# Kernel optimization log

Measured on AMD Instinct MI355X. Metric: run time of the kernel, lower is better.

## Reference

```python
import jax
jax.config.update("jax_enable_x64", True)
import jax.numpy as jnp
import numpy as np

# --- Field setup -------------------------------------------------------------
# The original uses BLS12-381 Fr (255-bit Montgomery limbs). JAX has no native
# 256-bit ints, so the reference uses an NTT-friendly 31-bit prime with the
# same algorithmic structure (two-adic radix-2 INTT, grand products, MSM-style
# commitment reduction). Products of two residues fit in int64.
P = 2013265921          # 15 * 2^27 + 1, two-adicity 27
G = 31                  # generator of F_P^*
LOG_N = 20
N = 1 << LOG_N
W = pow(G, (P - 1) // N, P)      # primitive N-th root of unity
W_INV = pow(W, P - 2, P)
N_INV = pow(N, P - 2, P)
K1, K2, K3 = 7, 13, 17           # PLONK coset shifts for wire identities


def _bitrev_perm(n):
    logn = n.bit_length() - 1
    idx = np.arange(n, dtype=np.int64)
    rev = np.zeros(n, dtype=np.int64)
    for i in range(logn):
        rev = (rev << 1) | ((idx >> i) & 1)
    return rev


def _twiddles(n, root):
    logn = n.bit_length() - 1
    out = []
    for s in range(1, logn + 1):
        m = 1 << s
        wm = pow(root, n // m, P)
        half = m >> 1
        ws = np.empty(half, dtype=np.int64)
        w = 1
        for k in range(half):
            ws[k] = w
            w = (w * wm) % P
        out.append(jnp.asarray(ws))
    return out

_BREV = jnp.asarray(_bitrev_perm(N))
_TW_INV = _twiddles(N, W_INV)


def _ntt_core(a, tw):
    # iterative radix-2 Cooley-Tukey, fully vectorized per stage
    n = a.shape[0]
    a = a[_BREV]
    for s, ws in enumerate(tw):
        half = 1 << s
        a = a.reshape(-1, 2 * half)         # [n/(2*half), 2*half]
        u = a[:, :half]
        t = (a[:, half:] * ws[None, :]) % P
        a = jnp.concatenate([(u + t) % P, (u - t) % P], axis=1)
    return a.reshape(n)


def intt(evals):
    # inverse NTT: evaluations on the domain -> coefficients (nn.Intt)
    return (_ntt_core(evals, _TW_INV) * N_INV) % P


def inv_mod(x):
    # batch modular inverse: x^(P-2), exponent is a compile-time constant
    e = P - 2
    res = jnp.ones_like(x)
    base = x % P
    while e:
        if e & 1:
            res = (res * base) % P
        base = (base * base) % P
        e >>= 1
    return res


def cumprod_mod(x):
    return jax.lax.associative_scan(lambda a, b: (a * b) % P, x)


def shifted_cumprod(r):
    # z[0] = 1, z[i] = prod_{j<i} r[j]
    c = cumprod_mod(r)
    return jnp.concatenate([jnp.ones((1,), r.dtype), c[:-1]])


def commit(poly, ck):
    # stand-in for the KZG MSM: <poly, ck> mod P (same reduction structure)
    return jnp.sum((poly * ck) % P) % P


def perm_z(wires, sigmas, beta, gamma, omega_pows):
    # PLONK copy-constraint grand product (mod.compute_permutation_poly)
    ids = (omega_pows, (K1 * omega_pows) % P,
           (K2 * omega_pows) % P, (K3 * omega_pows) % P)
    num = jnp.ones((N,), jnp.int64)
    den = jnp.ones((N,), jnp.int64)
    for w, i, s in zip(wires, ids, sigmas):
        num = (num * ((w + (beta * i) % P + gamma) % P)) % P
        den = (den * ((w + (beta * s) % P + gamma) % P)) % P
    return shifted_cumprod((num * inv_mod(den)) % P)


def lookup_z2(f, t, h1, h2, delta, epsilon):
    # plookup grand product (mod.compute_lookup_permutation_poly)
    one_plus_d = (1 + delta) % P
    ep1d = (epsilon * one_plus_d) % P
    t_next = jnp.roll(t, -1)
    h1_next = jnp.roll(h1, -1)
    h2_next = jnp.roll(h2, -1)
    num = (one_plus_d * ((epsilon + f) % P)) % P
    num = (num * ((ep1d + t + (delta * t_next) % P) % P)) % P
    a = (ep1d + h1 + (delta * h1_next) % P) % P
    b = (ep1d + h2 + (delta * h2_next) % P) % P
    den = (a * b) % P
    return shifted_cumprod((num * inv_mod(den)) % P)


def setup_inputs() -> dict:
    key = jax.random.key(0)
    ks = jax.random.split(key, 16)
    def ri(k):
        return jax.random.randint(k, (N,), 0, P, dtype=jnp.int64)
    return {
        "w_l": ri(ks[0]), "w_r": ri(ks[1]), "w_o": ri(ks[2]), "w_4": ri(ks[3]),
        "q_lookup": jax.random.randint(ks[4], (N,), 0, 2, dtype=jnp.int64),
        "t1": ri(ks[5]), "t2": ri(ks[6]), "t3": ri(ks[7]), "t4": ri(ks[8]),
        "sigma_l": ri(ks[9]), "sigma_r": ri(ks[10]),
        "sigma_o": ri(ks[11]), "sigma_4": ri(ks[12]),
        "ck": ri(ks[13]),
        "zeta": 123457, "beta": 98765, "gamma": 54321,
        "delta": 13579, "epsilon": 24680,
    }


def reference(w_l, w_r, w_o, w_4, q_lookup, t1, t2, t3, t4,
              sigma_l, sigma_r, sigma_o, sigma_4, ck,
              zeta, beta, gamma, delta, epsilon):
    z2c = (zeta * zeta) % P
    z3c = (z2c * zeta) % P
    # zkp.compress: zeta-combine lookup table columns
    t = (t1 + (zeta * t2) % P + (z2c * t3) % P + (z3c * t4) % P) % P
    table_poly = intt(t)
    # zkp.compute_query_table: compressed wire query where selector is on,
    # padded with table values where it is off
    q = (w_l + (zeta * w_r) % P + (z2c * w_o) % P + (z3c * w_4) % P) % P
    f = jnp.where(q_lookup == 1, q, t)
    f_poly = intt(f)
    # witness INTTs
    w_l_poly = intt(w_l)
    w_r_poly = intt(w_r)
    w_o_poly = intt(w_o)
    w_4_poly = intt(w_4)
    # combine_split: sorted multiset of f union t, split alternating
    s = jnp.sort(jnp.concatenate([f, t]))
    h1, h2 = s[0::2], s[1::2]
    h1_poly = intt(h1)
    h2_poly = intt(h2)
    # domain elements 1, W, W^2, ...
    omega_pows = shifted_cumprod(jnp.full((N,), W, dtype=jnp.int64))
    z = perm_z((w_l, w_r, w_o, w_4), (sigma_l, sigma_r, sigma_o, sigma_4),
               beta, gamma, omega_pows)
    z_poly = intt(z)
    z2 = lookup_z2(f, t, h1, h2, delta, epsilon)
    z2_poly = intt(z2)
    polys = (w_l_poly, w_r_poly, w_o_poly, w_4_poly, f_poly, table_poly,
             h1_poly, h2_poly, z_poly, z2_poly)
    commits = jnp.stack([commit(p, ck) for p in polys])
    return polys + (commits,)
```

## Files before the change

kernel.cpp:

```cpp
#include <hip/hip_runtime.h>
#include <stdint.h>

#define PRIME 2013265921u
#define LOGN  20
#define NN    (1u << LOGN)

static constexpr uint64_t cpowmod(uint64_t b, uint64_t e){
  uint64_t r = 1; b %= PRIME;
  while (e){ if (e & 1) r = r * b % PRIME; b = b * b % PRIME; e >>= 1; }
  return r;
}
static constexpr uint32_t WFWD = (uint32_t)cpowmod(31u, (PRIME - 1u) >> LOGN);
static constexpr uint32_t WINV = (uint32_t)cpowmod(WFWD, PRIME - 2u);
static constexpr uint32_t NINV = (uint32_t)cpowmod(NN, PRIME - 2u);
static constexpr uint64_t MBAR = 0xFFFFFFFFFFFFFFFFull / PRIME;

__device__ uint32_t g_U[1024];
__device__ uint32_t g_V[1024];
__device__ uint2    g_TWp[1024];
__device__ uint2    g_U2p[1024];
__device__ uint32_t g_bcnt[2048];
__device__ uint32_t g_boff[2048];
__device__ uint32_t g_bcur[2048];
__device__ uint32_t g_btot[2048];
__device__ uint32_t g_bpre[2048];
__device__ unsigned long long g_commit[10];

__device__ __forceinline__ uint32_t mulmod(uint32_t a, uint32_t b){
  uint64_t t = (uint64_t)a * b;
  uint32_t q = (uint32_t)__umul64hi(t, MBAR);
  uint32_t r = (uint32_t)t - q * PRIME;
  if (r >= PRIME) r -= PRIME;
  return r;
}
__device__ __forceinline__ uint32_t shoup_mul(uint32_t a, uint32_t w, uint32_t ws){
  uint32_t q = __umulhi(a, ws);
  uint32_t r = a * w - q * PRIME;
  if (r >= PRIME) r -= PRIME;
  return r;
}
__device__ __forceinline__ uint32_t addmod(uint32_t a, uint32_t b){
  uint32_t s = a + b; return (s >= PRIME) ? s - PRIME : s;
}
__device__ __forceinline__ uint32_t submod(uint32_t a, uint32_t b){
  return (a >= b) ? (a - b) : (a + (PRIME - b));
}
__device__ __forceinline__ uint32_t addmod3(uint32_t a, uint32_t b, uint32_t c){
  return addmod(addmod(a, b), c);
}
__device__ __forceinline__ uint32_t powmod_dev(uint32_t b, uint32_t e){
  uint32_t r = 1u;
  while (e){ if (e & 1u) r = mulmod(r, b); b = mulmod(b, b); e >>= 1u; }
  return r;
}

__global__ __launch_bounds__(1024) void k_zero(){
  const uint32_t t = blockIdx.x * 1024u + threadIdx.x;
  if (t < 2048u) g_bcnt[t] = 0u;
  if (t < 10u)   g_commit[t] = 0ull;
}

__global__ __launch_bounds__(1024) void k_tables(){
  const uint32_t i = threadIdx.x;
  if (blockIdx.x == 0){
    g_U[i] = powmod_dev(WINV, i);
  } else if (blockIdx.x == 1){
    g_V[i] = powmod_dev(WINV, i << 10);
  } else if (blockIdx.x == 2){
    const uint32_t w = mulmod(NINV, powmod_dev(WINV, i));
    g_U2p[i] = make_uint2(w, (uint32_t)((((uint64_t)w) << 32) / PRIME));
  } else {
    uint32_t j;
    if      (i < 512u)  j = i;
    else if (i < 768u)  j = (i - 512u)  << 1;
    else if (i < 896u)  j = (i - 768u)  << 2;
    else if (i < 960u)  j = (i - 896u)  << 3;
    else if (i < 992u)  j = (i - 960u)  << 4;
    else if (i < 1008u) j = (i - 992u)  << 5;
    else if (i < 1016u) j = (i - 1008u) << 6;
    else if (i < 1020u) j = (i - 1016u) << 7;
    else if (i < 1022u) j = (i - 1020u) << 8;
    else                j = 0u;
    const uint32_t w = powmod_dev(WINV, j << 10);
    g_TWp[i] = make_uint2(w, (uint32_t)((((uint64_t)w) << 32) / PRIME));
  }
}

__global__ __launch_bounds__(1024) void k_elemA(
    const uint32_t* __restrict__ wl, const uint32_t* __restrict__ wr,
    const uint32_t* __restrict__ wo, const uint32_t* __restrict__ w4,
    const uint32_t* __restrict__ ql, const uint32_t* __restrict__ x1,
    const uint32_t* __restrict__ x2, const uint32_t* __restrict__ x3,
    const uint32_t* __restrict__ x4, const uint32_t* __restrict__ zeta_p,
    uint32_t* __restrict__ o32)
{
  __shared__ uint32_t hcnt[2048];
  const int t = threadIdx.x;
  hcnt[t] = 0u; hcnt[t + 1024] = 0u;
  __syncthreads();

  const uint32_t zeta = zeta_p[0];
  const uint32_t zc2 = mulmod(zeta, zeta), zc3 = mulmod(zc2, zeta);
  const uint32_t i0 = (uint32_t)blockIdx.x * 4096u + (uint32_t)t * 4u;

  uint4 vt1 = *(const uint4*)(x1 + i0);
  uint4 vt2 = *(const uint4*)(x2 + i0);
  uint4 vt3 = *(const uint4*)(x3 + i0);
  uint4 vt4 = *(const uint4*)(x4 + i0);
  uint4 vwl = *(const uint4*)(wl + i0);
  uint4 vwr = *(const uint4*)(wr + i0);
  uint4 vwo = *(const uint4*)(wo + i0);
  uint4 vw4 = *(const uint4*)(w4 + i0);
  uint4 vql = *(const uint4*)(ql + i0);

  uint32_t T1[4] = {vt1.x, vt1.y, vt1.z, vt1.w};
  uint32_t T2[4] = {vt2.x, vt2.y, vt2.z, vt2.w};
  uint32_t T3[4] = {vt3.x, vt3.y, vt3.z, vt3.w};
  uint32_t T4[4] = {vt4.x, vt4.y, vt4.z, vt4.w};
  uint32_t L1[4] = {vwl.x, vwl.y, vwl.z, vwl.w};
  uint32_t L2[4] = {vwr.x, vwr.y, vwr.z, vwr.w};
  uint32_t L3[4] = {vwo.x, vwo.y, vwo.z, vwo.w};
  uint32_t L4[4] = {vw4.x, vw4.y, vw4.z, vw4.w};
  uint32_t QL[4] = {vql.x, vql.y, vql.z, vql.w};

  uint32_t tv[4], fv[4];
  #pragma unroll
  for (int k = 0; k < 4; ++k){
    uint32_t tt = addmod(addmod(T1[k], mulmod(zeta, T2[k])),
                         addmod(mulmod(zc2, T3[k]), mulmod(zc3, T4[k])));
    uint32_t qq = addmod(addmod(L1[k], mulmod(zeta, L2[k])),
                         addmod(mulmod(zc2, L3[k]), mulmod(zc3, L4[k])));
    tv[k] = tt; fv[k] = (QL[k] == 1u) ? qq : tt;
  }
  uint4 o;
  o.x = tv[0]; o.y = tv[1]; o.z = tv[2]; o.w = tv[3];
  *(uint4*)(o32 + 5u*NN + i0) = o;
  o.x = fv[0]; o.y = fv[1]; o.z = fv[2]; o.w = fv[3];
  *(uint4*)(o32 + 4u*NN + i0) = o;

  #pragma unroll
  for (int k = 0; k < 4; ++k){ atomicAdd(&hcnt[fv[k] >> 20], 1u);
                               atomicAdd(&hcnt[tv[k] >> 20], 1u); }
  __syncthreads();
  uint32_t c0 = hcnt[t];          if (c0) atomicAdd(&g_bcnt[t], c0);
  uint32_t c1 = hcnt[t + 1024];   if (c1) atomicAdd(&g_bcnt[t + 1024], c1);
}

__global__ __launch_bounds__(1024) void k_bscan(){
  __shared__ uint32_t SA[2048], SB[2048];
  const int t = threadIdx.x;
  SA[t] = g_bcnt[t];
  SA[t + 1024] = g_bcnt[t + 1024];
  __syncthreads();
  uint32_t* sp = SA; uint32_t* dp = SB;
  for (int off = 1; off < 2048; off <<= 1){
    for (int i = t; i < 2048; i += 1024)
      dp[i] = (i >= off) ? (sp[i - off] + sp[i]) : sp[i];
    uint32_t* tmp = sp; sp = dp; dp = tmp;
    __syncthreads();
  }
  uint32_t e0 = t ? sp[t - 1] : 0u;
  uint32_t e1 = sp[t + 1023];
  g_boff[t] = e0;         g_bcur[t] = e0;
  g_boff[t + 1024] = e1;  g_bcur[t + 1024] = e1;
}

__global__ __launch_bounds__(1024) void k_scat2(uint32_t* __restrict__ o32){
  __shared__ uint32_t sorted[8192];
  __shared__ uint32_t hist[2048];
  __shared__ uint32_t SA[2048];
  __shared__ uint32_t wsum[16];
  __shared__ uint32_t gbase[2048];
  const int t = threadIdx.x;
  const uint32_t base = blockIdx.x * 8192u;

  hist[t] = 0u; hist[t + 1024] = 0u;
  __syncthreads();

  uint32_t v[8], rk[8];
  #pragma unroll
  for (int k = 0; k < 8; ++k)
    v[k] = o32[4u*NN + base + (uint32_t)t + (uint32_t)k * 1024u];
  #pragma unroll
  for (int k = 0; k < 8; ++k)
    rk[k] = atomicAdd(&hist[v[k] >> 20], 1u);
  __syncthreads();

  const uint32_t lane = (uint32_t)t & 63u, wid = (uint32_t)t >> 6;
  const uint32_t e0 = hist[2*t], e1 = hist[2*t + 1];
  const uint32_t s = e0 + e1;
  uint32_t scan = s;
  #pragma unroll
  for (int off = 1; off < 64; off <<= 1){
    uint32_t u = __shfl_up(scan, off, 64);
    if (lane >= (uint32_t)off) scan += u;
  }
  if (lane == 63u) wsum[wid] = scan;
  __syncthreads();
  if (t < 64){
    uint32_t u = (t < 16) ? wsum[t] : 0u;
    #pragma unroll
    for (int off = 1; off < 16; off <<= 1){
      uint32_t x2 = __shfl_up(u, off, 64);
      if ((uint32_t)t >= (uint32_t)off) u += x2;
    }
    if (t < 16) wsum[t] = u;
  }
  __syncthreads();
  const uint32_t wbase = wid ? wsum[wid - 1] : 0u;
  const uint32_t incl = wbase + scan;
  SA[2*t]     = incl - e1;
  SA[2*t + 1] = incl;
  __syncthreads();
  uint32_t* sp = SA;

  for (int b = t; b < 2048; b += 1024){
    uint32_t c = hist[b];
    if (c) gbase[b] = atomicAdd(&g_bcur[b], c);
  }
  __syncthreads();

  #pragma unroll
  for (int k = 0; k < 8; ++k){
    uint32_t b = v[k] >> 20;
    uint32_t ls = b ? sp[b - 1] : 0u;
    sorted[ls + rk[k]] = v[k];
  }
  __syncthreads();

  for (int i = t; i < 8192; i += 1024){
    uint32_t vv = sorted[i];
    uint32_t b = vv >> 20;
    uint32_t ls = b ? sp[b - 1] : 0u;
    o32[6u*NN + gbase[b] + (uint32_t)i - ls] = vv;
  }
}

__global__ __launch_bounds__(256) void k_bsort(uint32_t* __restrict__ o32){
  __shared__ uint32_t sorted[2048];
  __shared__ uint32_t SA[1024], SB[1024];
  __shared__ uint32_t wsum[4];
  const int b = blockIdx.x, t = threadIdx.x;
  uint32_t n = g_bcnt[b]; if (n > 2048u) n = 2048u;
  const uint32_t off = g_boff[b];

  for (int i = t; i < 1024; i += 256) SA[i] = 0u;
  __syncthreads();

  uint32_t v[8], rk[8];
  #pragma unroll
  for (int k = 0; k < 8; ++k){
    const uint32_t i = (uint32_t)t + (uint32_t)k * 256u;
    if (i < n){
      v[k] = o32[6u*NN + off + i];
      rk[k] = atomicAdd(&SA[(v[k] >> 10) & 1023u], 1u);
    }
  }
  __syncthreads();

  const uint32_t lane = (uint32_t)t & 63u, wid = (uint32_t)t >> 6;
  const uint32_t h0 = SA[4*t], h1 = SA[4*t + 1], h2 = SA[4*t + 2], h3 = SA[4*t + 3];
  const uint32_t s = h0 + h1 + h2 + h3;
  uint32_t scan = s;
  #pragma unroll
  for (int o = 1; o < 64; o <<= 1){
    uint32_t u = __shfl_up(scan, o, 64);
    if (lane >= (uint32_t)o) scan += u;
  }
  if (lane == 63u) wsum[wid] = scan;
  __syncthreads();
  if (t < 64){
    uint32_t u = (t < 4) ? wsum[t] : 0u;
    #pragma unroll
    for (int o = 1; o < 4; o <<= 1){
      uint32_t x2 = __shfl_up(u, o, 64);
      if ((uint32_t)t >= (uint32_t)o) u += x2;
    }
    if (t < 4) wsum[t] = u;
  }
  __syncthreads();
  const uint32_t wbase = wid ? wsum[wid - 1] : 0u;
  const uint32_t incl = wbase + scan;
  SB[4*t + 3] = incl;
  SB[4*t + 2] = incl - h3;
  SB[4*t + 1] = incl - h3 - h2;
  SB[4*t + 0] = incl - h3 - h2 - h1;
  __syncthreads();
  uint32_t* sp = SB;

  #pragma unroll
  for (int k = 0; k < 8; ++k){
    const uint32_t i = (uint32_t)t + (uint32_t)k * 256u;
    if (i < n){
      const uint32_t d = (v[k] >> 10) & 1023u;
      const uint32_t s2 = d ? sp[d - 1] : 0u;
      sorted[s2 + rk[k]] = v[k];
    }
  }
  __syncthreads();

  for (int d = t; d < 1024; d += 256){
    const uint32_t s2 = d ? sp[d - 1] : 0u;
    const uint32_t e = sp[d];
    for (uint32_t i = s2 + 1; i < e; ++i){
      const uint32_t key = sorted[i];
      uint32_t j = i;
      while (j > s2 && sorted[j - 1] > key){ sorted[j] = sorted[j - 1]; --j; }
      sorted[j] = key;
    }
  }
  __syncthreads();

  for (uint32_t i = (uint32_t)t; i < n; i += 256u) o32[6u*NN + off + i] = sorted[i];
}

__global__ __launch_bounds__(256) void k_ratio(
    const uint32_t* __restrict__ wl, const uint32_t* __restrict__ wr,
    const uint32_t* __restrict__ wo, const uint32_t* __restrict__ w4,
    const uint32_t* __restrict__ sl, const uint32_t* __restrict__ sr,
    const uint32_t* __restrict__ so, const uint32_t* __restrict__ s4,
    const uint32_t* __restrict__ beta_p, const uint32_t* __restrict__ gamma_p,
    const uint32_t* __restrict__ delta_p, const uint32_t* __restrict__ eps_p,
    uint32_t* __restrict__ o32)
{
  __shared__ uint32_t SA[256], SB[256];
  const int blk = blockIdx.x, t = threadIdx.x;
  const int second = blk >> 9;
  const uint32_t base = ((uint32_t)(blk & 511) << 11) + ((uint32_t)t << 3);
  uint32_t num[8], den[8];
  if (!second){
    const uint32_t beta = beta_p[0], gamma = gamma_p[0];
    #pragma unroll
    for (int k = 0; k < 8; ++k){
      uint32_t i = base + (uint32_t)k;
      uint32_t e = (NN - i) & (NN - 1u);
      uint32_t om = mulmod(g_U[e & 1023u], g_V[e >> 10]);
      uint32_t bo = mulmod(beta, om);
      uint32_t n = addmod3(wl[i], bo, gamma);
      n = mulmod(n, addmod3(wr[i], mulmod(7u,  bo), gamma));
      n = mulmod(n, addmod3(wo[i], mulmod(13u, bo), gamma));
      n = mulmod(n, addmod3(w4[i], mulmod(17u, bo), gamma));
      uint32_t d = addmod3(wl[i], mulmod(beta, sl[i]), gamma);
      d = mulmod(d, addmod3(wr[i], mulmod(beta, sr[i]), gamma));
      d = mulmod(d, addmod3(wo[i], mulmod(beta, so[i]), gamma));
      d = mulmod(d, addmod3(w4[i], mulmod(beta, s4[i]), gamma));
      num[k] = n; den[k] = d;
    }
  } else {
    const uint32_t del = delta_p[0], ep = eps_p[0];
    const uint32_t opd = addmod(1u, del), ep1d = mulmod(ep, opd);
    #pragma unroll
    for (int k = 0; k < 8; ++k){
      uint32_t i = base + (uint32_t)k;
      uint32_t fi = o32[4u*NN + i], ti = o32[5u*NN + i];
      uint32_t tn = o32[5u*NN + ((i + 1u) & (NN - 1u))];
      uint32_t h1  = o32[6u*NN + 2u*i];
      uint32_t h2  = o32[6u*NN + 2u*i + 1u];
      uint32_t h1n = o32[6u*NN + ((2u*i + 2u) & (2u*NN - 1u))];
      uint32_t h2n = o32[6u*NN + ((2u*i + 3u) & (2u*NN - 1u))];
      uint32_t n = mulmod(opd, addmod(ep, fi));
      n = mulmod(n, addmod3(ep1d, ti, mulmod(del, tn)));
      uint32_t d = mulmod(addmod3(ep1d, h1, mulmod(del, h1n)),
                          addmod3(ep1d, h2, mulmod(del, h2n)));
      num[k] = n; den[k] = d;
    }
  }
  bool ok = true;
  #pragma unroll
  for (int k = 0; k < 8; ++k) ok = ok && (den[k] != 0u);
  uint32_t r[8];
  if (ok){
    uint32_t pp[8];
    pp[0] = den[0];
    #pragma unroll
    for (int k = 1; k < 8; ++k) pp[k] = mulmod(pp[k-1], den[k]);
    uint32_t iv = powmod_dev(pp[7], PRIME - 2u);
    #pragma unroll
    for (int k = 7; k >= 1; --k){
      r[k] = mulmod(num[k], mulmod(iv, pp[k-1]));
      iv = mulmod(iv, den[k]);
    }
    r[0] = mulmod(num[0], iv);
  } else {
    #pragma unroll
    for (int k = 0; k < 8; ++k) r[k] = mulmod(num[k], powmod_dev(den[k], PRIME - 2u));
  }
  uint32_t tp = r[0];
  #pragma unroll
  for (int k = 1; k < 8; ++k) tp = mulmod(tp, r[k]);
  SA[t] = tp; __syncthreads();
  uint32_t* sp = SA; uint32_t* dp = SB;
  for (int off = 1; off < 256; off <<= 1){
    dp[t] = (t >= off) ? mulmod(sp[t - off], sp[t]) : sp[t];
    uint32_t* tmp = sp; sp = dp; dp = tmp;
    __syncthreads();
  }
  if (t == 255) g_btot[blk] = sp[255];
  uint32_t run = t ? sp[t - 1] : 1u;
  const uint32_t zo = 8u*NN + ((uint32_t)second << 20) + base;
  #pragma unroll
  for (int k = 0; k < 8; ++k){
    o32[zo + (uint32_t)k] = run;
    run = mulmod(run, r[k]);
  }
}

__global__ __launch_bounds__(512) void k_btscan(){
  __shared__ uint32_t SA[512], SB[512];
  const int a = blockIdx.x, t = threadIdx.x;
  SA[t] = g_btot[a * 512 + t];
  __syncthreads();
  uint32_t* sp = SA; uint32_t* dp = SB;
  for (int off = 1; off < 512; off <<= 1){
    dp[t] = (t >= off) ? mulmod(sp[t - off], sp[t]) : sp[t];
    uint32_t* tmp = sp; sp = dp; dp = tmp;
    __syncthreads();
  }
  g_bpre[a * 512 + t] = t ? sp[t - 1] : 1u;
}

__global__ __launch_bounds__(256) void k_apply(uint32_t* __restrict__ o32){
  const uint32_t g = blockIdx.x * 256u + threadIdx.x;
  const uint32_t base = g << 2;
  const uint32_t m = g_bpre[base >> 11];
  uint4* zz = (uint4*)(o32 + 8u*NN);
  uint4 v = zz[g];
  v.x = mulmod(v.x, m); v.y = mulmod(v.y, m); v.z = mulmod(v.z, m); v.w = mulmod(v.w, m);
  zz[g] = v;
}

struct Desc  { const uint32_t* p; uint32_t stride; uint32_t off; };
struct Descs { Desc d[10]; };
struct Map   { int g[10]; };

#define SWZ(i, c) (((i) << 4) + ((c) ^ (((i) >> 1) & 15)))

__device__ __forceinline__ void ntt1024_reg(uint32_t x[16], int l,
                                            const uint2* __restrict__ sTW){
  #pragma unroll
  for (int st = 9; st >= 6; --st){
    const int bb = 1 << (st - 6);
    const int base = (st == 9) ? 0 : (st == 8) ? 512 : (st == 7) ? 768 : 896;
    #pragma unroll
    for (int r = 0; r < 16; ++r){
      if ((r & bb) == 0){
        const int r2 = r | bb;
        const uint32_t u = x[r], v = x[r2];
        const uint2 wv = sTW[base + ((r & (bb - 1)) << 6) + l];
        x[r]  = addmod(u, v);
        x[r2] = shoup_mul(submod(u, v), wv.x, wv.y);
      }
    }
  }
  #pragma unroll
  for (int st = 5; st >= 0; --st){
    const int h = 1 << st;
    const int base = (st == 5) ? 960 : (st == 4) ? 992 : (st == 3) ? 1008
                   : (st == 2) ? 1016 : (st == 1) ? 1020 : 1022;
    const uint2 wv = sTW[base + (l & (h - 1))];
    const bool hi = (l & h) != 0;
    #pragma unroll
    for (int r = 0; r < 16; ++r){
      const uint32_t y = __shfl_xor(x[r], h, 64);
      const uint32_t a = addmod(x[r], y);
      const uint32_t b = shoup_mul(submod(y, x[r]), wv.x, wv.y);
      x[r] = hi ? b : a;
    }
  }
}

__global__ __launch_bounds__(1024, 8) void k_intt1(Descs ds, uint32_t* __restrict__ mid){
  __shared__ uint32_t tile[16384];
  __shared__ uint2 sTW[1024];
  const int arr = blockIdx.x >> 6;
  const int c0 = (blockIdx.x & 63) << 4;
  const Desc de = ds.d[arr];
  const int t = threadIdx.x;
  sTW[t] = g_TWp[t];
  if (de.stride == 1u){
    #pragma unroll
    for (int it = 0; it < 4; ++it){
      const int row = (it << 8) + (t >> 2);
      const int cb = (t & 3) << 2;
      uint4 v = *(const uint4*)(de.p + (size_t)row * 1024u + (uint32_t)(c0 + cb));
      tile[SWZ(row, cb + 0)] = v.x; tile[SWZ(row, cb + 1)] = v.y;
      tile[SWZ(row, cb + 2)] = v.z; tile[SWZ(row, cb + 3)] = v.w;
    }
  } else {
    #pragma unroll
    for (int it = 0; it < 4; ++it){
      const int row = (it << 8) + (t >> 2);
      const int cb = (t & 3) << 2;
      const size_t b0 = 2u * ((size_t)row * 1024u + (uint32_t)(c0 + cb));
      uint4 a0 = *(const uint4*)(de.p + b0);
      uint4 a1 = *(const uint4*)(de.p + b0 + 4u);
      if (de.off == 0u){
        tile[SWZ(row, cb + 0)] = a0.x; tile[SWZ(row, cb + 1)] = a0.z;
        tile[SWZ(row, cb + 2)] = a1.x; tile[SWZ(row, cb + 3)] = a1.z;
      } else {
        tile[SWZ(row, cb + 0)] = a0.y; tile[SWZ(row, cb + 1)] = a0.w;
        tile[SWZ(row, cb + 2)] = a1.y; tile[SWZ(row, cb + 3)] = a1.w;
      }
    }
  }
  __syncthreads();
  const int w = t >> 6, l = t & 63;
  uint32_t x[16];
  #pragma unroll
  for (int r = 0; r < 16; ++r) x[r] = tile[SWZ(l + (r << 6), w)];
  ntt1024_reg(x, l, sTW);
  const uint32_t i1g = (uint32_t)(c0 + w);
  const uint32_t rl = __brev((uint32_t)l) >> 26;
  #pragma unroll
  for (int r = 0; r < 16; ++r){
    const uint32_t rr = __brev((uint32_t)r) >> 28;
    const uint32_t j1 = (rl << 4) | rr;
    const uint32_t e = j1 * i1g;
    const uint2 wa = g_U2p[e & 1023u];
    const uint32_t hv = e >> 10;
    const uint2 wb = sTW[hv & 511u];
    uint32_t wbw = wb.x, wbs = wb.y;
    if (hv & 512u){ wbw = PRIME - wbw; wbs = ~wbs; }
    x[r] = shoup_mul(x[r], wa.x, wa.y);
    x[r] = shoup_mul(x[r], wbw, wbs);
  }
  __syncthreads();
  #pragma unroll
  for (int r = 0; r < 16; ++r) tile[SWZ(l + (r << 6), w)] = x[r];
  __syncthreads();
  uint32_t* mo = mid + ((size_t)arr << 20);
  #pragma unroll
  for (int it = 0; it < 4; ++it){
    const int row = (it << 8) + (t >> 2);
    const int cb = (t & 3) << 2;
    uint4 v;
    v.x = tile[SWZ(row, cb + 0)]; v.y = tile[SWZ(row, cb + 1)];
    v.z = tile[SWZ(row, cb + 2)]; v.w = tile[SWZ(row, cb + 3)];
    *(uint4*)(mo + (size_t)row * 1024u + (uint32_t)(c0 + cb)) = v;
  }
}

__global__ __launch_bounds__(1024, 8) void k_intt2(const uint32_t* __restrict__ mid,
                                                   uint32_t* __restrict__ o32,
                                                   const uint32_t* __restrict__ ck,
                                                   Map mp){
  __shared__ uint32_t tile[16384];
  __shared__ uint2 sTW[1024];
  const int arrL = blockIdx.x >> 6;
  const int m0 = (blockIdx.x & 63) << 4;
  const int t = threadIdx.x;
  const int w = t >> 6, l = t & 63;
  const int gidx = mp.g[arrL];
  const uint32_t* mi = mid + ((size_t)arrL << 20);
  const uint32_t p = __brev((uint32_t)(m0 + w)) >> 22;
  sTW[t] = g_TWp[t];
  #pragma unroll
  for (int it = 0; it < 4; ++it){
    const int kb = (it << 8) + (l << 2);
    uint4 v = *(const uint4*)(mi + p * 1024u + (uint32_t)kb);
    tile[SWZ(kb + 0, w)] = v.x; tile[SWZ(kb + 1, w)] = v.y;
    tile[SWZ(kb + 2, w)] = v.z; tile[SWZ(kb + 3, w)] = v.w;
  }
  __syncthreads();
  uint32_t x[16];
  #pragma unroll
  for (int r = 0; r < 16; ++r) x[r] = tile[SWZ(l + (r << 6), w)];
  ntt1024_reg(x, l, sTW);
  __syncthreads();
  #pragma unroll
  for (int r = 0; r < 16; ++r) tile[SWZ(l + (r << 6), w)] = x[r];
  __syncthreads();
  unsigned long long acc = 0ull;
  uint32_t* oa = o32 + ((size_t)gidx << 20);
  #pragma unroll
  for (int it = 0; it < 4; ++it){
    const int j2 = (it << 8) + (t >> 2);
    const int rb = (t & 3) << 2;
    const uint32_t q = __brev((uint32_t)j2) >> 22;
    uint4 v;
    v.x = tile[SWZ((int)q, rb + 0)]; v.y = tile[SWZ((int)q, rb + 1)];
    v.z = tile[SWZ((int)q, rb + 2)]; v.w = tile[SWZ((int)q, rb + 3)];
    const uint32_t oi = (uint32_t)j2 * 1024u + (uint32_t)(m0 + rb);
    *(uint4*)(oa + oi) = v;
    uint4 cv = *(const uint4*)(ck + oi);
    acc += (unsigned long long)mulmod(v.x, cv.x);
    acc += (unsigned long long)mulmod(v.y, cv.y);
    acc += (unsigned long long)mulmod(v.z, cv.z);
    acc += (unsigned long long)mulmod(v.w, cv.w);
  }
  #pragma unroll
  for (int off = 32; off >= 1; off >>= 1) acc += __shfl_down(acc, off, 64);
  __syncthreads();
  unsigned long long* redw = (unsigned long long*)tile;
  if (l == 0) redw[w] = acc;
  __syncthreads();
  if (t < 64){
    unsigned long long s = (t < 16) ? redw[t] : 0ull;
    #pragma unroll
    for (int off = 8; off >= 1; off >>= 1) s += __shfl_down(s, off, 64);
    if (t == 0) atomicAdd(&g_commit[gidx], s);
  }
}

__global__ __launch_bounds__(256) void k_brev(const uint32_t* __restrict__ src,
                                              uint32_t stride, uint32_t off,
                                              uint32_t* __restrict__ dst){
  const uint32_t i = blockIdx.x * 256u + threadIdx.x;
  const uint32_t r = __brev(i) >> 12;
  dst[i] = src[(size_t)r * stride + off];
}

__global__ __launch_bounds__(1024) void k_stage09(uint32_t* __restrict__ wk){
  __shared__ uint32_t sm[1024];
  const int t = threadIdx.x;
  const uint32_t gbase = blockIdx.x * 1024u;
  sm[t] = wk[gbase + t];
  __syncthreads();
  for (int s = 0; s <= 9; ++s){
    if (t < 512){
      const int half = 1 << s;
      const int k = t & (half - 1);
      const int i0 = ((t >> s) << (s + 1)) | k;
      const int i1 = i0 + half;
      const uint32_t tw = g_V[(uint32_t)k << (9 - s)];
      const uint32_t u = sm[i0];
      const uint32_t tv = mulmod(sm[i1], tw);
      sm[i0] = addmod(u, tv);
      sm[i1] = submod(u, tv);
    }
    __syncthreads();
  }
  wk[gbase + t] = sm[t];
}

__global__ __launch_bounds__(256) void k_stage(uint32_t* __restrict__ wk, int s){
  const uint32_t q = blockIdx.x * 256u + threadIdx.x;
  const uint32_t half = 1u << s;
  const uint32_t k = q & (half - 1u);
  const uint32_t i0 = ((q >> s) << (s + 1)) | k;
  const uint32_t i1 = i0 + half;
  const uint32_t e = k << (19 - s);
  const uint32_t tw = mulmod(g_U[e & 1023u], g_V[e >> 10]);
  const uint32_t u = wk[i0];
  const uint32_t tv = mulmod(wk[i1], tw);
  wk[i0] = addmod(u, tv);
  wk[i1] = submod(u, tv);
}

__global__ __launch_bounds__(1024) void k_scale_commit(const uint32_t* __restrict__ src,
                                                       uint32_t* dst,
                                                       const uint32_t* __restrict__ ck,
                                                       int cidx){
  __shared__ unsigned long long red[1024];
  const uint32_t i = blockIdx.x * 1024u + threadIdx.x;
  const uint32_t val = mulmod(src[i], NINV);
  dst[i] = val;
  red[threadIdx.x] = (unsigned long long)mulmod(val, ck[i]);
  __syncthreads();
  for (int s = 512; s > 0; s >>= 1){
    if ((int)threadIdx.x < s) red[threadIdx.x] += red[threadIdx.x + s];
    __syncthreads();
  }
  if (threadIdx.x == 0) atomicAdd(&g_commit[cidx], red[0]);
}

__global__ void k_final(uint32_t* __restrict__ out){
  const int i = threadIdx.x;
  if (i < 10) out[(size_t)10 * NN + i] = (uint32_t)(g_commit[i] % (unsigned long long)PRIME);
}

extern "C" void kernel_launch(void* const* d_in, const int* in_sizes, int n_in,
                              void* d_out, int out_size, void* d_ws, size_t ws_size,
                              hipStream_t stream)
{
  const uint32_t* wl   = (const uint32_t*)d_in[0];
  const uint32_t* wr   = (const uint32_t*)d_in[1];
  const uint32_t* wo   = (const uint32_t*)d_in[2];
  const uint32_t* w4   = (const uint32_t*)d_in[3];
  const uint32_t* ql   = (const uint32_t*)d_in[4];
  const uint32_t* t1   = (const uint32_t*)d_in[5];
  const uint32_t* t2   = (const uint32_t*)d_in[6];
  const uint32_t* t3   = (const uint32_t*)d_in[7];
  const uint32_t* t4   = (const uint32_t*)d_in[8];
  const uint32_t* sl   = (const uint32_t*)d_in[9];
  const uint32_t* sr   = (const uint32_t*)d_in[10];
  const uint32_t* so   = (const uint32_t*)d_in[11];
  const uint32_t* s4   = (const uint32_t*)d_in[12];
  const uint32_t* ck   = (const uint32_t*)d_in[13];
  const uint32_t* zeta = (const uint32_t*)d_in[14];
  const uint32_t* beta = (const uint32_t*)d_in[15];
  const uint32_t* gam  = (const uint32_t*)d_in[16];
  const uint32_t* del  = (const uint32_t*)d_in[17];
  const uint32_t* eps  = (const uint32_t*)d_in[18];
  uint32_t* o32 = (uint32_t*)d_out;
  (void)in_sizes; (void)n_in; (void)out_size;

  k_zero  <<<2, 1024, 0, stream>>>();
  k_tables<<<4, 1024, 0, stream>>>();
  k_elemA <<<256, 1024, 0, stream>>>(wl, wr, wo, w4, ql, t1, t2, t3, t4, zeta, o32);
  k_bscan <<<1, 1024, 0, stream>>>();
  k_scat2 <<<256, 1024, 0, stream>>>(o32);
  k_bsort <<<1920, 256, 0, stream>>>(o32);
  k_ratio <<<1024, 256, 0, stream>>>(wl, wr, wo, w4, sl, sr, so, s4, beta, gam, del, eps, o32);
  k_btscan<<<2, 512, 0, stream>>>();
  k_apply <<<2048, 256, 0, stream>>>(o32);

  Desc ds[10];
  ds[0] = { wl,          1u, 0u };
  ds[1] = { wr,          1u, 0u };
  ds[2] = { wo,          1u, 0u };
  ds[3] = { w4,          1u, 0u };
  ds[4] = { o32 + 4u*NN, 1u, 0u };
  ds[5] = { o32 + 5u*NN, 1u, 0u };
  ds[6] = { o32 + 6u*NN, 2u, 0u };
  ds[7] = { o32 + 6u*NN, 2u, 1u };
  ds[8] = { o32 + 8u*NN, 1u, 0u };
  ds[9] = { o32 + 9u*NN, 1u, 0u };

  const size_t wsWords = ws_size / 4u;
  if (wsWords >= 2ull * NN){
    static const int ord[10] = {6,7, 4,5, 8,9, 0,1, 2,3};
    const int chunk = (wsWords >= 10ull * NN) ? 10 : 2;
    uint32_t* mid = (uint32_t*)d_ws;
    for (int s0 = 0; s0 < 10; s0 += chunk){
      const int cnt = (10 - s0 < chunk) ? (10 - s0) : chunk;
      Descs sub; Map mp;
      for (int a = 0; a < 10; ++a){
        const int g = ord[(a < cnt) ? s0 + a : s0];
        sub.d[a] = ds[g]; mp.g[a] = g;
      }
      k_intt1<<<64 * cnt, 1024, 0, stream>>>(sub, mid);
      k_intt2<<<64 * cnt, 1024, 0, stream>>>(mid, o32, ck, mp);
    }
  } else {
    auto run_intt = [&](const Desc& d, uint32_t workSlot, int dstSlot){
      uint32_t* wk = o32 + (size_t)workSlot * NN;
      k_brev   <<<4096, 256, 0, stream>>>(d.p, d.stride, d.off, wk);
      k_stage09<<<1024, 1024, 0, stream>>>(wk);
      for (int s = 10; s < 20; ++s)
        k_stage<<<2048, 256, 0, stream>>>(wk, s);
      k_scale_commit<<<1024, 1024, 0, stream>>>(wk, o32 + (size_t)dstSlot * NN, ck, dstSlot);
    };
    k_brev<<<4096, 256, 0, stream>>>(ds[6].p, 2u, 0u, o32 + 0u*NN);
    k_brev<<<4096, 256, 0, stream>>>(ds[7].p, 2u, 1u, o32 + 1u*NN);
    {
      uint32_t* wk0 = o32;
      uint32_t* wk1 = o32 + NN;
      k_stage09<<<1024, 1024, 0, stream>>>(wk0);
      for (int s = 10; s < 20; ++s) k_stage<<<2048, 256, 0, stream>>>(wk0, s);
      k_scale_commit<<<1024, 1024, 0, stream>>>(wk0, o32 + 6u*NN, ck, 6);
      k_stage09<<<1024, 1024, 0, stream>>>(wk1);
      for (int s = 10; s < 20; ++s) k_stage<<<2048, 256, 0, stream>>>(wk1, s);
      k_scale_commit<<<1024, 1024, 0, stream>>>(wk1, o32 + 7u*NN, ck, 7);
    }
    run_intt(ds[4], 0u, 4);
    run_intt(ds[5], 1u, 5);
    run_intt(ds[8], 0u, 8);
    run_intt(ds[9], 1u, 9);
    run_intt(ds[0], 0u, 0);
    run_intt(ds[1], 1u, 1);
    run_intt(ds[2], 2u, 2);
    run_intt(ds[3], 3u, 3);
  }
  k_final<<<1, 64, 0, stream>>>(o32);
}
```

Measured before the change: 200.0 us.

## Halve NTT block size: each thread processes two columns with half-size LDS tile

The two four-step NTT kernels now launch 512 threads instead of 1024. Each wave handles two 1024-point columns held in registers (xA/xB), and the shared tile shrinks from 64KB to 32KB, staged in two halves. The goal is to cut LDS footprint so more blocks fit per CU, and to expose more independent work per thread so latency is better hidden. In exchange, register pressure doubles, which could reduce occupancy, and the extra half-staging passes add barriers.

Result: slower. 215.5 us (+7.7%).

```diff
diff --git a/kernel.cpp b/kernel.cpp
--- a/kernel.cpp
+++ b/kernel.cpp
@@ -435,8 +435,8 @@
 
 #define SWZ(i, c) (((i) << 4) + ((c) ^ (((i) >> 1) & 15)))
 
-__device__ __forceinline__ void ntt1024_reg(uint32_t x[16], int l,
-                                            const uint2* __restrict__ sTW){
+__device__ __forceinline__ void ntt1024_reg2(uint32_t xA[16], uint32_t xB[16], int l,
+                                             const uint2* __restrict__ sTW){
   #pragma unroll
   for (int st = 9; st >= 6; --st){
     const int bb = 1 << (st - 6);
@@ -445,10 +445,13 @@
     for (int r = 0; r < 16; ++r){
       if ((r & bb) == 0){
         const int r2 = r | bb;
-        const uint32_t u = x[r], v = x[r2];
         const uint2 wv = sTW[base + ((r & (bb - 1)) << 6) + l];
-        x[r]  = addmod(u, v);
-        x[r2] = shoup_mul(submod(u, v), wv.x, wv.y);
+        const uint32_t uA = xA[r], vA = xA[r2];
+        xA[r]  = addmod(uA, vA);
+        xA[r2] = shoup_mul(submod(uA, vA), wv.x, wv.y);
+        const uint32_t uB = xB[r], vB = xB[r2];
+        xB[r]  = addmod(uB, vB);
+        xB[r2] = shoup_mul(submod(uB, vB), wv.x, wv.y);
       }
     }
   }
@@ -461,132 +464,191 @@
     const bool hi = (l & h) != 0;
     #pragma unroll
     for (int r = 0; r < 16; ++r){
-      const uint32_t y = __shfl_xor(x[r], h, 64);
-      const uint32_t a = addmod(x[r], y);
-      const uint32_t b = shoup_mul(submod(y, x[r]), wv.x, wv.y);
-      x[r] = hi ? b : a;
-    }
-  }
-}
-
-__global__ __launch_bounds__(1024, 8) void k_intt1(Descs ds, uint32_t* __restrict__ mid){
-  __shared__ uint32_t tile[16384];
+      const uint32_t yA = __shfl_xor(xA[r], h, 64);
+      const uint32_t aA = addmod(xA[r], yA);
+      const uint32_t bA = shoup_mul(submod(yA, xA[r]), wv.x, wv.y);
+      xA[r] = hi ? bA : aA;
+      const uint32_t yB = __shfl_xor(xB[r], h, 64);
+      const uint32_t aB = addmod(xB[r], yB);
+      const uint32_t bB = shoup_mul(submod(yB, xB[r]), wv.x, wv.y);
+      xB[r] = hi ? bB : aB;
+    }
+  }
+}
+
+__global__ __launch_bounds__(512, 8) void k_intt1(Descs ds, uint32_t* __restrict__ mid){
+  __shared__ uint32_t tile[8192];
   __shared__ uint2 sTW[1024];
+  const int t = threadIdx.x;
+  sTW[t] = g_TWp[t];
+  sTW[t + 512] = g_TWp[t + 512];
   const int arr = blockIdx.x >> 6;
   const int c0 = (blockIdx.x & 63) << 4;
   const Desc de = ds.d[arr];
+  const int w = t >> 6, l = t & 63;
+  uint32_t xA[16], xB[16];
+
+  #pragma unroll
+  for (int H = 0; H < 2; ++H){
+    if (H) __syncthreads();
+    if (de.stride == 1u){
+      #pragma unroll
+      for (int it = 0; it < 4; ++it){
+        const int rl = (it << 7) + (t >> 2);
+        const int cb = (t & 3) << 2;
+        const int row = (H << 9) + rl;
+        uint4 v = *(const uint4*)(de.p + (size_t)row * 1024u + (uint32_t)(c0 + cb));
+        tile[SWZ(rl, cb + 0)] = v.x; tile[SWZ(rl, cb + 1)] = v.y;
+        tile[SWZ(rl, cb + 2)] = v.z; tile[SWZ(rl, cb + 3)] = v.w;
+      }
+    } else {
+      #pragma unroll
+      for (int it = 0; it < 4; ++it){
+        const int rl = (it << 7) + (t >> 2);
+        const int cb = (t & 3) << 2;
+        const int row = (H << 9) + rl;
+        const size_t b0 = 2u * ((size_t)row * 1024u + (uint32_t)(c0 + cb));
+        uint4 a0 = *(const uint4*)(de.p + b0);
+        uint4 a1 = *(const uint4*)(de.p + b0 + 4u);
+        if (de.off == 0u){
+          tile[SWZ(rl, cb + 0)] = a0.x; tile[SWZ(rl, cb + 1)] = a0.z;
+          tile[SWZ(rl, cb + 2)] = a1.x; tile[SWZ(rl, cb + 3)] = a1.z;
+        } else {
+          tile[SWZ(rl, cb + 0)] = a0.y; tile[SWZ(rl, cb + 1)] = a0.w;
+          tile[SWZ(rl, cb + 2)] = a1.y; tile[SWZ(rl, cb + 3)] = a1.w;
+        }
+      }
+    }
+    __syncthreads();
+    #pragma unroll
+    for (int r = 0; r < 8; ++r){
+      const int rl = l + (r << 6);
+      xA[(H << 3) + r] = tile[SWZ(rl, w)];
+      xB[(H << 3) + r] = tile[SWZ(rl, w + 8)];
+    }
+  }
+  ntt1024_reg2(xA, xB, l, sTW);
+  const uint32_t i1gA = (uint32_t)(c0 + w);
+  const uint32_t i1gB = (uint32_t)(c0 + w + 8);
+  const uint32_t rl6 = __brev((uint32_t)l) >> 26;
+  #pragma unroll
+  for (int r = 0; r < 16; ++r){
+    const uint32_t rr = __brev((uint32_t)r) >> 28;
+    const uint32_t j1 = (rl6 << 4) | rr;
+    {
+      const uint32_t e = j1 * i1gA;
+      const uint2 wa = g_U2p[e & 1023u];
+      const uint32_t hv = e >> 10;
+      const uint2 wb = sTW[hv & 511u];
+      uint32_t wbw = wb.x, wbs = wb.y;
+      if (hv & 512u){ wbw = PRIME - wbw; wbs = ~wbs; }
+      xA[r] = shoup_mul(shoup_mul(xA[r], wa.x, wa.y), wbw, wbs);
+    }
+    {
+      const uint32_t e = j1 * i1gB;
+      const uint2 wa = g_U2p[e & 1023u];
+      const uint32_t hv = e >> 10;
+      const uint2 wb = sTW[hv & 511u];
+      uint32_t wbw = wb.x, wbs = wb.y;
+      if (hv & 512u){ wbw = PRIME - wbw; wbs = ~wbs; }
+      xB[r] = shoup_mul(shoup_mul(xB[r], wa.x, wa.y), wbw, wbs);
+    }
+  }
+  uint32_t* mo = mid + ((size_t)arr << 20);
+  #pragma unroll
+  for (int H = 0; H < 2; ++H){
+    __syncthreads();
+    #pragma unroll
+    for (int r = 0; r < 8; ++r){
+      const int rl = l + (r << 6);
+      tile[SWZ(rl, w)]     = xA[(H << 3) + r];
+      tile[SWZ(rl, w + 8)] = xB[(H << 3) + r];
+    }
+    __syncthreads();
+    #pragma unroll
+    for (int it = 0; it < 4; ++it){
+      const int rl = (it << 7) + (t >> 2);
+      const int cb = (t & 3) << 2;
+      const int row = (H << 9) + rl;
+      uint4 v;
+      v.x = tile[SWZ(rl, cb + 0)]; v.y = tile[SWZ(rl, cb + 1)];
+      v.z = tile[SWZ(rl, cb + 2)]; v.w = tile[SWZ(rl, cb + 3)];
+      *(uint4*)(mo + (size_t)row * 1024u + (uint32_t)(c0 + cb)) = v;
+    }
+  }
+}
+
+__global__ __launch_bounds__(512, 8) void k_intt2(const uint32_t* __restrict__ mid,
+                                                  uint32_t* __restrict__ o32,
+                                                  const uint32_t* __restrict__ ck,
+                                                  Map mp){
+  __shared__ uint32_t tile[8192];
+  __shared__ uint2 sTW[1024];
   const int t = threadIdx.x;
   sTW[t] = g_TWp[t];
-  if (de.stride == 1u){
-    #pragma unroll
-    for (int it = 0; it < 4; ++it){
-      const int row = (it << 8) + (t >> 2);
-      const int cb = (t & 3) << 2;
-      uint4 v = *(const uint4*)(de.p + (size_t)row * 1024u + (uint32_t)(c0 + cb));
-      tile[SWZ(row, cb + 0)] = v.x; tile[SWZ(row, cb + 1)] = v.y;
-      tile[SWZ(row, cb + 2)] = v.z; tile[SWZ(row, cb + 3)] = v.w;
-    }
-  } else {
-    #pragma unroll
-    for (int it = 0; it < 4; ++it){
-      const int row = (it << 8) + (t >> 2);
-      const int cb = (t & 3) << 2;
-      const size_t b0 = 2u * ((size_t)row * 1024u + (uint32_t)(c0 + cb));
-      uint4 a0 = *(const uint4*)(de.p + b0);
-      uint4 a1 = *(const uint4*)(de.p + b0 + 4u);
-      if (de.off == 0u){
-        tile[SWZ(row, cb + 0)] = a0.x; tile[SWZ(row, cb + 1)] = a0.z;
-        tile[SWZ(row, cb + 2)] = a1.x; tile[SWZ(row, cb + 3)] = a1.z;
-      } else {
-        tile[SWZ(row, cb + 0)] = a0.y; tile[SWZ(row, cb + 1)] = a0.w;
-        tile[SWZ(row, cb + 2)] = a1.y; tile[SWZ(row, cb + 3)] = a1.w;
-      }
-    }
-  }
-  __syncthreads();
-  const int w = t >> 6, l = t & 63;
-  uint32_t x[16];
-  #pragma unroll
-  for (int r = 0; r < 16; ++r) x[r] = tile[SWZ(l + (r << 6), w)];
-  ntt1024_reg(x, l, sTW);
-  const uint32_t i1g = (uint32_t)(c0 + w);
-  const uint32_t rl = __brev((uint32_t)l) >> 26;
-  #pragma unroll
-  for (int r = 0; r < 16; ++r){
-    const uint32_t rr = __brev((uint32_t)r) >> 28;
-    const uint32_t j1 = (rl << 4) | rr;
-    const uint32_t e = j1 * i1g;
-    const uint2 wa = g_U2p[e & 1023u];
-    const uint32_t hv = e >> 10;
-    const uint2 wb = sTW[hv & 511u];
-    uint32_t wbw = wb.x, wbs = wb.y;
-    if (hv & 512u){ wbw = PRIME - wbw; wbs = ~wbs; }
-    x[r] = shoup_mul(x[r], wa.x, wa.y);
-    x[r] = shoup_mul(x[r], wbw, wbs);
-  }
-  __syncthreads();
-  #pragma unroll
-  for (int r = 0; r < 16; ++r) tile[SWZ(l + (r << 6), w)] = x[r];
-  __syncthreads();
-  uint32_t* mo = mid + ((size_t)arr << 20);
-  #pragma unroll
-  for (int it = 0; it < 4; ++it){
-    const int row = (it << 8) + (t >> 2);
-    const int cb = (t & 3) << 2;
-    uint4 v;
-    v.x = tile[SWZ(row, cb + 0)]; v.y = tile[SWZ(row, cb + 1)];
-    v.z = tile[SWZ(row, cb + 2)]; v.w = tile[SWZ(row, cb + 3)];
-    *(uint4*)(mo + (size_t)row * 1024u + (uint32_t)(c0 + cb)) = v;
-  }
-}
-
-__global__ __launch_bounds__(1024, 8) void k_intt2(const uint32_t* __restrict__ mid,
-                                                   uint32_t* __restrict__ o32,
-                                                   const uint32_t* __restrict__ ck,
-                                                   Map mp){
-  __shared__ uint32_t tile[16384];
-  __shared__ uint2 sTW[1024];
+  sTW[t + 512] = g_TWp[t + 512];
   const int arrL = blockIdx.x >> 6;
   const int m0 = (blockIdx.x & 63) << 4;
-  const int t = threadIdx.x;
   const int w = t >> 6, l = t & 63;
   const int gidx = mp.g[arrL];
   const uint32_t* mi = mid + ((size_t)arrL << 20);
-  const uint32_t p = __brev((uint32_t)(m0 + w)) >> 22;
-  sTW[t] = g_TWp[t];
-  #pragma unroll
-  for (int it = 0; it < 4; ++it){
-    const int kb = (it << 8) + (l << 2);
-    uint4 v = *(const uint4*)(mi + p * 1024u + (uint32_t)kb);
-    tile[SWZ(kb + 0, w)] = v.x; tile[SWZ(kb + 1, w)] = v.y;
-    tile[SWZ(kb + 2, w)] = v.z; tile[SWZ(kb + 3, w)] = v.w;
-  }
-  __syncthreads();
-  uint32_t x[16];
-  #pragma unroll
-  for (int r = 0; r < 16; ++r) x[r] = tile[SWZ(l + (r << 6), w)];
-  ntt1024_reg(x, l, sTW);
-  __syncthreads();
-  #pragma unroll
-  for (int r = 0; r < 16; ++r) tile[SWZ(l + (r << 6), w)] = x[r];
-  __syncthreads();
+  const uint32_t pA = __brev((uint32_t)(m0 + w)) >> 22;
+  const uint32_t pB = __brev((uint32_t)(m0 + w + 8)) >> 22;
+  uint32_t xA[16], xB[16];
+
+  #pragma unroll
+  for (int H = 0; H < 2; ++H){
+    if (H) __syncthreads();
+    #pragma unroll
+    for (int it = 0; it < 2; ++it){
+      const int kb = (it << 8) + (l << 2);
+      const int k2 = (H << 9) + kb;
+      uint4 v = *(const uint4*)(mi + pA * 1024u + (uint32_t)k2);
+      tile[SWZ(kb + 0, w)] = v.x; tile[SWZ(kb + 1, w)] = v.y;
+      tile[SWZ(kb + 2, w)] = v.z; tile[SWZ(kb + 3, w)] = v.w;
+      uint4 u = *(const uint4*)(mi + pB * 1024u + (uint32_t)k2);
+      tile[SWZ(kb + 0, w + 8)] = u.x; tile[SWZ(kb + 1, w + 8)] = u.y;
+      tile[SWZ(kb + 2, w + 8)] = u.z; tile[SWZ(kb + 3, w + 8)] = u.w;
+    }
+    __syncthreads();
+    #pragma unroll
+    for (int r = 0; r < 8; ++r){
+      const int rl = l + (r << 6);
+      xA[(H << 3) + r] = tile[SWZ(rl, w)];
+      xB[(H << 3) + r] = tile[SWZ(rl, w + 8)];
+    }
+  }
+  ntt1024_reg2(xA, xB, l, sTW);
   unsigned long long acc = 0ull;
   uint32_t* oa = o32 + ((size_t)gidx << 20);
   #pragma unroll
-  for (int it = 0; it < 4; ++it){
-    const int j2 = (it << 8) + (t >> 2);
-    const int rb = (t & 3) << 2;
-    const uint32_t q = __brev((uint32_t)j2) >> 22;
-    uint4 v;
-    v.x = tile[SWZ((int)q, rb + 0)]; v.y = tile[SWZ((int)q, rb + 1)];
-    v.z = tile[SWZ((int)q, rb + 2)]; v.w = tile[SWZ((int)q, rb + 3)];
-    const uint32_t oi = (uint32_t)j2 * 1024u + (uint32_t)(m0 + rb);
-    *(uint4*)(oa + oi) = v;
-    uint4 cv = *(const uint4*)(ck + oi);
-    acc += (unsigned long long)mulmod(v.x, cv.x);
-    acc += (unsigned long long)mulmod(v.y, cv.y);
-    acc += (unsigned long long)mulmod(v.z, cv.z);
-    acc += (unsigned long long)mulmod(v.w, cv.w);
+  for (int H = 0; H < 2; ++H){
+    __syncthreads();
+    #pragma unroll
+    for (int r = 0; r < 8; ++r){
+      const int rl = l + (r << 6);
+      tile[SWZ(rl, w)]     = xA[(H << 3) + r];
+      tile[SWZ(rl, w + 8)] = xB[(H << 3) + r];
+    }
+    __syncthreads();
+    #pragma unroll
+    for (int it = 0; it < 4; ++it){
+      const int m = (it << 7) + (t >> 2);
+      const int j2 = (m << 1) | H;
+      const uint32_t q = __brev((uint32_t)j2) >> 22;
+      const int ql = (int)(q & 511u);
+      const int rb = (t & 3) << 2;
+      uint4 v;
+      v.x = tile[SWZ(ql, rb + 0)]; v.y = tile[SWZ(ql, rb + 1)];
+      v.z = tile[SWZ(ql, rb + 2)]; v.w = tile[SWZ(ql, rb + 3)];
+      const uint32_t oi = (uint32_t)j2 * 1024u + (uint32_t)(m0 + rb);
+      *(uint4*)(oa + oi) = v;
+      uint4 cv = *(const uint4*)(ck + oi);
+      acc += (unsigned long long)mulmod(v.x, cv.x);
+      acc += (unsigned long long)mulmod(v.y, cv.y);
+      acc += (unsigned long long)mulmod(v.z, cv.z);
+      acc += (unsigned long long)mulmod(v.w, cv.w);
+    }
   }
   #pragma unroll
   for (int off = 32; off >= 1; off >>= 1) acc += __shfl_down(acc, off, 64);
@@ -595,9 +657,9 @@
   if (l == 0) redw[w] = acc;
   __syncthreads();
   if (t < 64){
-    unsigned long long s = (t < 16) ? redw[t] : 0ull;
-    #pragma unroll
-    for (int off = 8; off >= 1; off >>= 1) s += __shfl_down(s, off, 64);
+    unsigned long long s = (t < 8) ? redw[t] : 0ull;
+    #pragma unroll
+    for (int off = 4; off >= 1; off >>= 1) s += __shfl_down(s, off, 64);
     if (t == 0) atomicAdd(&g_commit[gidx], s);
   }
 }
@@ -729,8 +791,8 @@
         const int g = ord[(a < cnt) ? s0 + a : s0];
         sub.d[a] = ds[g]; mp.g[a] = g;
       }
-      k_intt1<<<64 * cnt, 1024, 0, stream>>>(sub, mid);
-      k_intt2<<<64 * cnt, 1024, 0, stream>>>(mid, o32, ck, mp);
+      k_intt1<<<64 * cnt, 512, 0, stream>>>(sub, mid);
+      k_intt2<<<64 * cnt, 512, 0, stream>>>(mid, o32, ck, mp);
     }
   } else {
     auto run_intt = [&](const Desc& d, uint32_t workSlot, int dstSlot){
```
